# Kernel optimization log

Measured on AMD Instinct MI355X. Metric: run time of the kernel, lower is better.

Reference implementation:

```python
import jax, jax.numpy as jnp
import numpy as np

T_STEPS, B, DX, DH = 512, 64, 1024, 1024


def setup_inputs() -> dict:
    key = jax.random.key(0)
    ks = jax.random.split(key, 8)
    s_in = 1.0 / np.sqrt(DX)
    s_h = 1.0 / np.sqrt(DH)
    return {
        "xs": jax.random.normal(ks[0], (T_STEPS, B, DX), jnp.float32),
        "ms": jax.random.normal(ks[1], (T_STEPS, B, DH), jnp.float32),
        "h0": jnp.zeros((B, DH), jnp.float32),
        "W_ih": jax.random.normal(ks[2], (3 * DH, DX), jnp.float32) * s_in,
        "b_ih": jnp.zeros((3 * DH,), jnp.float32),
        "W_hh": jax.random.normal(ks[3], (3 * DH, DH), jnp.float32) * s_h,
        "b_hh": jnp.zeros((3 * DH,), jnp.float32),
        "W_xh": jax.random.normal(ks[4], (DH, DX), jnp.float32) * s_in,
        "b_xh": jnp.zeros((DH,), jnp.float32),
        "W_r": jax.random.normal(ks[5], (DH, DH), jnp.float32) * s_h,
        "b_r": jnpp if False else jnp.zeros((DH,), jnp.float32),
    }


def reference(xs, ms, h0, W_ih, b_ih, W_hh, b_hh, W_xh, b_xh, W_r, b_r):
    # Precompute all input-side projections in one big GEMM each (same math,
    # just hoisted out of the recurrent loop).
    xg = jnp.einsum('tbd,gd->tbg', xs, W_ih) + b_ih          # [T,B,3*Dh]
    xh = jnp.einsum('tbd,hd->tbh', xs, W_xh) + b_xh          # [T,B,Dh]
    tm = jnp.tanh(ms)                                        # [T,B,Dh]

    def step(h, inp):
        xg_t, xh_t, tm_t = inp
        hg = h @ W_hh.T + b_hh                               # [B,3*Dh]
        gates = jax.nn.sigmoid(xg_t + hg)
        rt, zt, et = jnp.split(gates, 3, axis=-1)
        ht_hat = jnp.tanh(xh_t + (rt * h) @ W_r.T + b_r)
        ht = zt * h + (1.0 - zt) * ht_hat + et * tm_t
        return ht, ht

    h_last, outs = jax.lax.scan(step, h0, (xg, xh, tm))
    return outs, h_last
```

## Files before the change

### kernel.cpp

```cpp
#include <hip/hip_runtime.h>
#include <stdint.h>

#define TSTEPS 512

typedef __attribute__((ext_vector_type(8))) _Float16 half8;
typedef __attribute__((ext_vector_type(4))) _Float16 half4;
typedef __attribute__((ext_vector_type(4))) float f32x4;
typedef __attribute__((ext_vector_type(4))) float float4v;
typedef __attribute__((ext_vector_type(4))) int i32x4;
typedef unsigned long long u64;

static __device__ __forceinline__ float sigm(float x) { return 1.f / (1.f + __expf(-x)); }
static __device__ __forceinline__ float tanh_(float x) {
  x = fminf(15.f, fmaxf(-15.f, x));
  float e = __expf(-2.f * x);
  return (1.f - e) / (1.f + e);
}
static __device__ __forceinline__ half8 ld8(const _Float16* p) { return *(const half8*)p; }
static __device__ __forceinline__ f32x4 MFMA(half8 a, half8 b, f32x4 c) {
  return __builtin_amdgcn_mfma_f32_16x16x32_f16(a, b, c, 0, 0, 0);
}
static __device__ __forceinline__ void pin8(half8& v) {
  i32x4 t = __builtin_bit_cast(i32x4, v);
  asm volatile("" : "+v"(t));
  v = __builtin_bit_cast(half8, t);
}

struct U64x2 { u64 x, y; };
static __device__ __forceinline__ half8 ld_msg16(const u64* p) {
  u64 a = __hip_atomic_load(p,     __ATOMIC_RELAXED, __HIP_MEMORY_SCOPE_AGENT);
  u64 b = __hip_atomic_load(p + 1, __ATOMIC_RELAXED, __HIP_MEMORY_SCOPE_AGENT);
  U64x2 u{a, b};
  return __builtin_bit_cast(half8, u);
}
static __device__ __forceinline__ void st_msg(u64* p, u64 v) {
  __hip_atomic_store(p, v, __ATOMIC_RELAXED, __HIP_MEMORY_SCOPE_AGENT);
}
static __device__ __forceinline__ void wait_flags(const unsigned* line, unsigned tag) {
  const unsigned* p = line + (threadIdx.x & 31);
  while (!__all(__hip_atomic_load(p, __ATOMIC_RELAXED, __HIP_MEMORY_SCOPE_AGENT) >= tag))
    __builtin_amdgcn_s_sleep(1);
  asm volatile("" ::: "memory");
}

__global__ __launch_bounds__(256) void kconv(
    const float* __restrict__ xs, const float* __restrict__ wih,
    const float* __restrict__ wxh, const float* __restrict__ whhf,
    const float* __restrict__ wrf, const float* __restrict__ h0,
    _Float16* __restrict__ xs_h, _Float16* __restrict__ wcat,
    _Float16* __restrict__ whh, _Float16* __restrict__ wr,
    _Float16* __restrict__ hx) {
  const long n1 = 8388608;
  const long n2 = 1048576;
  const long n3 = 786432;
  const long n4 = 262144;
  const long n5 = 16384;
  const long total = n1 + n2 + n3 + n4 + n5;
  for (long i = (long)blockIdx.x * 256 + threadIdx.x; i < total; i += (long)gridDim.x * 256) {
    const float* s; _Float16* d;
    if (i < n1) { s = xs + i * 4; d = xs_h + i * 4; }
    else if (i < n1 + n2) {
      long e = (i - n1) * 4;
      s = (e < 3145728) ? (wih + e) : (wxh + (e - 3145728));
      d = wcat + e;
    } else if (i < n1 + n2 + n3) { long e = (i - n1 - n2) * 4; s = whhf + e; d = whh + e; }
    else if (i < n1 + n2 + n3 + n4) { long e = (i - n1 - n2 - n3) * 4; s = wrf + e; d = wr + e; }
    else { long e = (i - n1 - n2 - n3 - n4) * 4; s = h0 + e; d = hx + e; }
    float4v v = *(const float4v*)s;
    half4 o = { (_Float16)v.x, (_Float16)v.y, (_Float16)v.z, (_Float16)v.w };
    *(half4*)d = o;
  }
}

__global__ __launch_bounds__(256) void kgemm(
    const _Float16* __restrict__ X, const _Float16* __restrict__ W,
    const float* __restrict__ b_ih, const float* __restrict__ b_xh,
    _Float16* __restrict__ C) {
  __shared__ _Float16 As[128 * 40], Bs[128 * 40];
  const int tid = threadIdx.x;
  const int lane = tid & 63;
  const int w = tid >> 6;
  const int wm = (w >> 1) * 64, wn = (w & 1) * 64;
  const int bn = blockIdx.x * 128;
  const int bm = blockIdx.y * 128;
  const int arow = tid >> 2;
  const int kk8 = (tid & 3) * 8;
  const int fr = lane & 15, fq = lane >> 4;
  const f32x4 zero = {0.f, 0.f, 0.f, 0.f};
  f32x4 acc[4][4];
  #pragma unroll
  for (int a = 0; a < 4; a++)
    #pragma unroll
    for (int b = 0; b < 4; b++) acc[a][b] = zero;
  for (int kt = 0; kt < 1024; kt += 32) {
    __syncthreads();
    #pragma unroll
    for (int j = 0; j < 2; j++) {
      int r = j * 64 + arow;
      *(half8*)(As + r * 40 + kk8) = ld8(X + (size_t)(bm + r) * 1024 + kt + kk8);
      *(half8*)(Bs + r * 40 + kk8) = ld8(W + (size_t)(bn + r) * 1024 + kt + kk8);
    }
    __syncthreads();
    half8 af[4], bfr[4];
    #pragma unroll
    for (int i = 0; i < 4; i++) {
      af[i]  = *(const half8*)(As + (wm + i * 16 + fr) * 40 + fq * 8);
      bfr[i] = *(const half8*)(Bs + (wn + i * 16 + fr) * 40 + fq * 8);
    }
    #pragma unroll
    for (int mi = 0; mi < 4; mi++)
      #pragma unroll
      for (int ni = 0; ni < 4; ni++)
        acc[mi][ni] = MFMA(af[mi], bfr[ni], acc[mi][ni]);
  }
  #pragma unroll
  for (int mi = 0; mi < 4; mi++)
    #pragma unroll
    for (int ni = 0; ni < 4; ni++) {
      int col = bn + wn + ni * 16 + fr;
      float bias = (col < 3072) ? b_ih[col] : b_xh[col - 3072];
      #pragma unroll
      for (int r = 0; r < 4; r++) {
        int row = bm + wm + mi * 16 + fq * 4 + r;
        C[(size_t)row * 4096 + col] = (_Float16)(acc[mi][ni][r] + bias);
      }
    }
}

#define RP 20
#define TP (16 * RP)

__global__ __launch_bounds__(512, 2) void krec(
    const _Float16* __restrict__ xgh, const float* __restrict__ ms,
    const _Float16* __restrict__ whh, const _Float16* __restrict__ wr,
    const float* __restrict__ b_hh, const float* __restrict__ b_r,
    const float* __restrict__ h0,
    u64* __restrict__ hmsg, u64* __restrict__ rhmsg,
    float* __restrict__ out, unsigned* __restrict__ ctr) {
  __shared__ float red[48 * TP];
  const int tid = threadIdx.x;
  const int lane = tid & 63, w = tid >> 6;
  const int fr = lane & 15, fq = lane >> 4;
  const int g = (int)blockIdx.x >> 5;
  const int slot = (int)blockIdx.x & 31;
  const int colbase = slot * 32;
  unsigned* flagA = ctr + (g * 2 + 0) * 32;
  unsigned* flagB = ctr + (g * 2 + 1) * 32;

  half8 wA[6][4], wB[2][4];
  #pragma unroll
  for (int nt = 0; nt < 6; nt++)
    #pragma unroll
    for (int ks = 0; ks < 4; ks++)
      wA[nt][ks] = ld8(whh + (size_t)((nt >> 1) * 1024 + colbase + (nt & 1) * 16 + fr) * 1024
                            + w * 128 + ks * 32 + fq * 8);
  #pragma unroll
  for (int nt = 0; nt < 2; nt++)
    #pragma unroll
    for (int ks = 0; ks < 4; ks++)
      wB[nt][ks] = ld8(wr + (size_t)(colbase + nt * 16 + fr) * 1024
                           + w * 128 + ks * 32 + fq * 8);
  #pragma unroll
  for (int nt = 0; nt < 6; nt++)
    #pragma unroll
    for (int ks = 0; ks < 4; ks++) pin8(wA[nt][ks]);
  #pragma unroll
  for (int nt = 0; nt < 2; nt++)
    #pragma unroll
    for (int ks = 0; ks < 4; ks++) pin8(wB[nt][ks]);

  const int b = tid >> 5, cc = tid & 31;
  const int gc = colbase + cc;
  const int gm = g * 16 + b;
  const float bhr = b_hh[gc], bhz = b_hh[1024 + gc], bhe = b_hh[2048 + gc];
  const float brr = b_r[gc];
  float hreg = h0[(size_t)gm * 1024 + gc];

  const u64* hcons = hmsg  + (g * 16 + fr) * 256 + w * 32 + fq * 2;
  const u64* rcons = rhmsg + (g * 16 + fr) * 256 + w * 32 + fq * 2;
  u64* hprod = hmsg  + gm * 256 + (gc >> 2);
  u64* rprod = rhmsg + gm * 256 + (gc >> 2);

  const f32x4 zero = {0.f, 0.f, 0.f, 0.f};

  float pxr, pxz, pxe, pxh, ptm;
  {
    const _Float16* xp = xgh + (size_t)gm * 4096;
    pxr = (float)xp[gc]; pxz = (float)xp[1024 + gc];
    pxe = (float)xp[2048 + gc]; pxh = (float)xp[3072 + gc];
    ptm = tanh_(ms[(size_t)gm * 1024 + gc]);
  }

  #pragma clang loop unroll(disable)
  for (int t = 0; t < TSTEPS; t++) {
    const int ph = t & 1;
    wait_flags(flagB, (unsigned)t);
    half8 av[4];
    #pragma unroll
    for (int ks = 0; ks < 4; ks++)
      av[ks] = ld_msg16(hcons + ph * 16384 + ks * 8);
    f32x4 accA[6];
    #pragma unroll
    for (int nt = 0; nt < 6; nt++) accA[nt] = zero;
    #pragma unroll
    for (int ks = 0; ks < 4; ks++)
      #pragma unroll
      for (int nt = 0; nt < 6; nt++)
        accA[nt] = MFMA(av[ks], wA[nt][ks], accA[nt]);
    #pragma unroll
    for (int nt = 0; nt < 6; nt++)
      #pragma unroll
      for (int r = 0; r < 4; r++)
        red[(w * 6 + nt) * TP + (fq * 4 + r) * RP + fr] = accA[nt][r];
    __syncthreads();
    float sr = pxr + bhr, sz = pxz + bhz, se = pxe + bhe;
    {
      const int boff = b * RP + (cc & 15) + (cc >> 4) * TP;
      #pragma unroll
      for (int w8 = 0; w8 < 8; w8++) {
        const float* rp = red + w8 * 6 * TP + boff;
        sr += rp[0]; sz += rp[2 * TP]; se += rp[4 * TP];
      }
    }
    float rg = sigm(sr);
    float zz = sigm(sz), ee = sigm(se);
    {
      float rv = rg * hreg;
      unsigned us = (unsigned)(unsigned short)__builtin_bit_cast(unsigned short, (_Float16)rv);
      unsigned v01 = us | (((unsigned)__shfl_down((int)us, 1) & 0xFFFFu) << 16);
      unsigned v23 = (unsigned)__shfl_down((int)v01, 2);
      if (!(cc & 3))
        st_msg(rprod + ph * 16384, ((u64)v23 << 32) | (u64)v01);
    }
    asm volatile("s_waitcnt vmcnt(0)" ::: "memory");
    __syncthreads();
    if (tid == 0)
      __hip_atomic_store(flagA + slot, (unsigned)(t + 1),
                         __ATOMIC_RELAXED, __HIP_MEMORY_SCOPE_AGENT);
    float nxr = 0.f, nxz = 0.f, nxe = 0.f, nxh = 0.f, ntm = 0.f;
    if (t + 1 < TSTEPS) {
      const _Float16* xp = xgh + (size_t)((t + 1) * 64 + gm) * 4096;
      nxr = (float)xp[gc]; nxz = (float)xp[1024 + gc];
      nxe = (float)xp[2048 + gc]; nxh = (float)xp[3072 + gc];
      ntm = tanh_(ms[(size_t)(t + 1) * 65536 + gm * 1024 + gc]);
    }

    wait_flags(flagA, (unsigned)(t + 1));
    half8 bv[4];
    #pragma unroll
    for (int ks = 0; ks < 4; ks++)
      bv[ks] = ld_msg16(rcons + ph * 16384 + ks * 8);
    f32x4 accB[2];
    #pragma unroll
    for (int nt = 0; nt < 2; nt++) accB[nt] = zero;
    #pragma unroll
    for (int ks = 0; ks < 4; ks++)
      #pragma unroll
      for (int nt = 0; nt < 2; nt++)
        accB[nt] = MFMA(bv[ks], wB[nt][ks], accB[nt]);
    #pragma unroll
    for (int nt = 0; nt < 2; nt++)
      #pragma unroll
      for (int r = 0; r < 4; r++)
        red[(w * 6 + nt) * TP + (fq * 4 + r) * RP + fr] = accB[nt][r];
    __syncthreads();
    float s = pxh + brr;
    {
      const int boff = b * RP + (cc & 15) + (cc >> 4) * TP;
      #pragma unroll
      for (int w8 = 0; w8 < 8; w8++) s += red[w8 * 6 * TP + boff];
    }
    float hh = tanh_(s);
    float hn = zz * hreg + (1.f - zz) * hh + ee * ptm;
    hreg = hn;
    {
      unsigned us = (unsigned)(unsigned short)__builtin_bit_cast(unsigned short, (_Float16)hn);
      unsigned v01 = us | (((unsigned)__shfl_down((int)us, 1) & 0xFFFFu) << 16);
      unsigned v23 = (unsigned)__shfl_down((int)v01, 2);
      if (!(cc & 3))
        st_msg(hprod + (ph ^ 1) * 16384, ((u64)v23 << 32) | (u64)v01);
    }
    asm volatile("s_waitcnt vmcnt(0)" ::: "memory");
    __syncthreads();
    if (tid == 0)
      __hip_atomic_store(flagB + slot, (unsigned)(t + 1),
                         __ATOMIC_RELAXED, __HIP_MEMORY_SCOPE_AGENT);
    __builtin_nontemporal_store(hn, out + (size_t)t * 65536 + gm * 1024 + gc);
    pxr = nxr; pxz = nxz; pxe = nxe; pxh = nxh; ptm = ntm;
  }
  out[(size_t)TSTEPS * 65536 + gm * 1024 + gc] = hreg;
}

extern "C" void kernel_launch(void* const* d_in, const int* in_sizes, int n_in,
                              void* d_out, int out_size, void* d_ws, size_t ws_size,
                              hipStream_t stream) {
  const float* xs   = (const float*)d_in[0];
  const float* ms   = (const float*)d_in[1];
  const float* h0   = (const float*)d_in[2];
  const float* W_ih = (const float*)d_in[3];
  const float* b_ih = (const float*)d_in[4];
  const float* W_hh = (const float*)d_in[5];
  const float* b_hh = (const float*)d_in[6];
  const float* W_xh = (const float*)d_in[7];
  const float* b_xh = (const float*)d_in[8];
  const float* W_r  = (const float*)d_in[9];
  const float* b_r  = (const float*)d_in[10];

  char* ws = (char*)d_ws;
  size_t off = 0;
  _Float16* xs_h = (_Float16*)(ws + off); off += 67108864;
  _Float16* wcat = (_Float16*)(ws + off); off += 8388608;
  _Float16* whh  = (_Float16*)(ws + off); off += 6291456;
  _Float16* wr   = (_Float16*)(ws + off); off += 2097152;
  _Float16* xgh  = (_Float16*)(ws + off); off += 268435456;
  _Float16* hx   = (_Float16*)(ws + off); off += 262144;
  _Float16* rhx  = (_Float16*)(ws + off); off += 262144;
  unsigned* ctr  = (unsigned*)(ws + off); off += 1024;

  hipMemsetAsync(ctr, 0, 1024, stream);
  kconv<<<2048, 256, 0, stream>>>(xs, W_ih, W_xh, W_hh, W_r, h0,
                                  xs_h, wcat, whh, wr, hx);
  kgemm<<<dim3(32, 256), 256, 0, stream>>>(xs_h, wcat, b_ih, b_xh, xgh);
  krec<<<128, 512, 0, stream>>>(xgh, ms, whh, wr, b_hh, b_r, h0,
                                (u64*)hx, (u64*)rhx, (float*)d_out, ctr);
}
```

Measured before the change: 4.455 ms.

## Place recurrent groups by XCC and exchange state through L2 atomics

The recurrent kernel now launches 256 blocks. Each block reads its XCC id and registers per XCC, so each 32-block group sits on one XCC and can exchange hidden-state messages and flags through that XCC's local L2 using atomic swap/add instructions instead of agent-scope loads. A global 'truth' flag acts as a fallback, and if placement fails the kernel falls back to the old global path. The first step also reads h0 directly instead of converting it in kconv, and the register pinning of weights is removed. This aims to cut cross-XCC coherence latency per timestep, at the cost of a startup rendezvous, spin-loop complexity and reliance on hardware-specific placement.

```diff
diff --git a/kernel.cpp b/kernel.cpp
--- a/kernel.cpp
+++ b/kernel.cpp
@@ -20,42 +20,62 @@
 static __device__ __forceinline__ f32x4 MFMA(half8 a, half8 b, f32x4 c) {
   return __builtin_amdgcn_mfma_f32_16x16x32_f16(a, b, c, 0, 0, 0);
 }
-static __device__ __forceinline__ void pin8(half8& v) {
-  i32x4 t = __builtin_bit_cast(i32x4, v);
-  asm volatile("" : "+v"(t));
-  v = __builtin_bit_cast(half8, t);
-}
-
-struct U64x2 { u64 x, y; };
-static __device__ __forceinline__ half8 ld_msg16(const u64* p) {
-  u64 a = __hip_atomic_load(p,     __ATOMIC_RELAXED, __HIP_MEMORY_SCOPE_AGENT);
-  u64 b = __hip_atomic_load(p + 1, __ATOMIC_RELAXED, __HIP_MEMORY_SCOPE_AGENT);
-  U64x2 u{a, b};
-  return __builtin_bit_cast(half8, u);
-}
-static __device__ __forceinline__ void st_msg(u64* p, u64 v) {
+
+static __device__ __forceinline__ unsigned aadd(unsigned* p) {
+  return __hip_atomic_fetch_add(p, 1u, __ATOMIC_RELAXED, __HIP_MEMORY_SCOPE_AGENT);
+}
+static __device__ __forceinline__ unsigned ald(const unsigned* p) {
+  return __hip_atomic_load(p, __ATOMIC_RELAXED, __HIP_MEMORY_SCOPE_AGENT);
+}
+static __device__ __forceinline__ void ast(unsigned* p, unsigned v) {
   __hip_atomic_store(p, v, __ATOMIC_RELAXED, __HIP_MEMORY_SCOPE_AGENT);
 }
-static __device__ __forceinline__ void wait_flags(const unsigned* line, unsigned tag) {
-  const unsigned* p = line + (threadIdx.x & 31);
-  while (!__all(__hip_atomic_load(p, __ATOMIC_RELAXED, __HIP_MEMORY_SCOPE_AGENT) >= tag))
-    __builtin_amdgcn_s_sleep(1);
-  asm volatile("" ::: "memory");
+static __device__ __forceinline__ u64 ald64(const u64* p) {
+  return __hip_atomic_load(p, __ATOMIC_RELAXED, __HIP_MEMORY_SCOPE_AGENT);
+}
+static __device__ __forceinline__ void ast64(u64* p, u64 v) {
+  __hip_atomic_store(p, v, __ATOMIC_RELAXED, __HIP_MEMORY_SCOPE_AGENT);
+}
+
+static __device__ __forceinline__ void l2_st64(u64* p, u64 v) {
+  asm volatile("global_atomic_swap_x2 %0, %1, off" :: "v"(p), "v"(v) : "memory");
+}
+static __device__ __forceinline__ void l2_st32(unsigned* p, unsigned v) {
+  asm volatile("global_atomic_swap %0, %1, off" :: "v"(p), "v"(v) : "memory");
+}
+static __device__ __forceinline__ unsigned l2_ld32(const unsigned* p) {
+  unsigned r, z = 0;
+  asm volatile("global_atomic_add %0, %1, %2, off sc0\n\ts_waitcnt vmcnt(0)"
+               : "=&v"(r) : "v"(p), "v"(z) : "memory");
+  return r;
+}
+static __device__ __forceinline__ void l2_ld_frag(
+    const u64* p0, const u64* p1, const u64* p2, const u64* p3, u64* m) {
+  u64 z = 0;
+  asm volatile(
+    "global_atomic_add_x2 %0, %8, %12, off sc0\n\t"
+    "global_atomic_add_x2 %1, %8, %12, off offset:8 sc0\n\t"
+    "global_atomic_add_x2 %2, %9, %12, off sc0\n\t"
+    "global_atomic_add_x2 %3, %9, %12, off offset:8 sc0\n\t"
+    "global_atomic_add_x2 %4, %10, %12, off sc0\n\t"
+    "global_atomic_add_x2 %5, %10, %12, off offset:8 sc0\n\t"
+    "global_atomic_add_x2 %6, %11, %12, off sc0\n\t"
+    "global_atomic_add_x2 %7, %11, %12, off offset:8 sc0\n\t"
+    "s_waitcnt vmcnt(0)"
+    : "=&v"(m[0]), "=&v"(m[1]), "=&v"(m[2]), "=&v"(m[3]),
+      "=&v"(m[4]), "=&v"(m[5]), "=&v"(m[6]), "=&v"(m[7])
+    : "v"(p0), "v"(p1), "v"(p2), "v"(p3), "v"(z)
+    : "memory");
 }
 
 __global__ __launch_bounds__(256) void kconv(
     const float* __restrict__ xs, const float* __restrict__ wih,
     const float* __restrict__ wxh, const float* __restrict__ whhf,
-    const float* __restrict__ wrf, const float* __restrict__ h0,
+    const float* __restrict__ wrf,
     _Float16* __restrict__ xs_h, _Float16* __restrict__ wcat,
-    _Float16* __restrict__ whh, _Float16* __restrict__ wr,
-    _Float16* __restrict__ hx) {
-  const long n1 = 8388608;
-  const long n2 = 1048576;
-  const long n3 = 786432;
-  const long n4 = 262144;
-  const long n5 = 16384;
-  const long total = n1 + n2 + n3 + n4 + n5;
+    _Float16* __restrict__ whh, _Float16* __restrict__ wr) {
+  const long n1 = 8388608, n2 = 1048576, n3 = 786432, n4 = 262144;
+  const long total = n1 + n2 + n3 + n4;
   for (long i = (long)blockIdx.x * 256 + threadIdx.x; i < total; i += (long)gridDim.x * 256) {
     const float* s; _Float16* d;
     if (i < n1) { s = xs + i * 4; d = xs_h + i * 4; }
@@ -64,8 +84,7 @@
       s = (e < 3145728) ? (wih + e) : (wxh + (e - 3145728));
       d = wcat + e;
     } else if (i < n1 + n2 + n3) { long e = (i - n1 - n2) * 4; s = whhf + e; d = whh + e; }
-    else if (i < n1 + n2 + n3 + n4) { long e = (i - n1 - n2 - n3) * 4; s = wrf + e; d = wr + e; }
-    else { long e = (i - n1 - n2 - n3 - n4) * 4; s = h0 + e; d = hx + e; }
+    else { long e = (i - n1 - n2 - n3) * 4; s = wrf + e; d = wr + e; }
     float4v v = *(const float4v*)s;
     half4 o = { (_Float16)v.x, (_Float16)v.y, (_Float16)v.z, (_Float16)v.w };
     *(half4*)d = o;
@@ -130,22 +149,50 @@
 #define RP 20
 #define TP (16 * RP)
 
-__global__ __launch_bounds__(512, 2) void krec(
+template<int LOCAL>
+static __device__ __forceinline__ void waitf(
+    const unsigned* fl, unsigned ftag, const unsigned* tr, unsigned ttag) {
+  if (LOCAL) {
+    if ((threadIdx.x >> 6) == 0) {
+      const unsigned* p = fl + (threadIdx.x & 31);
+      const unsigned* q = tr + (threadIdx.x & 31);
+      int it = 0;
+      for (;;) {
+        if (__all(l2_ld32(p) >= ftag)) break;
+        ++it;
+        if ((it & 63) == 0) {
+          if (__all(ald(q) >= ttag)) break;
+          if (it > 200000) break;
+        }
+        __builtin_amdgcn_s_sleep(1);
+      }
+    }
+    __syncthreads();
+  } else {
+    const unsigned* q = tr + (threadIdx.x & 31);
+    while (!__all(ald(q) >= ttag))
+      __builtin_amdgcn_s_sleep(1);
+  }
+  asm volatile("" ::: "memory");
+}
+
+template<int LOCAL>
+static __device__ void run_rec(
+    int tid, int grp, int slot, unsigned base,
     const _Float16* __restrict__ xgh, const float* __restrict__ ms,
     const _Float16* __restrict__ whh, const _Float16* __restrict__ wr,
     const float* __restrict__ b_hh, const float* __restrict__ b_r,
     const float* __restrict__ h0,
-    u64* __restrict__ hmsg, u64* __restrict__ rhmsg,
-    float* __restrict__ out, unsigned* __restrict__ ctr) {
-  __shared__ float red[48 * TP];
-  const int tid = threadIdx.x;
+    u64* __restrict__ hx, u64* __restrict__ rhx,
+    unsigned* __restrict__ truth, unsigned* __restrict__ flagsL,
+    float* __restrict__ out, float* red) {
   const int lane = tid & 63, w = tid >> 6;
   const int fr = lane & 15, fq = lane >> 4;
-  const int g = (int)blockIdx.x >> 5;
-  const int slot = (int)blockIdx.x & 31;
   const int colbase = slot * 32;
-  unsigned* flagA = ctr + (g * 2 + 0) * 32;
-  unsigned* flagB = ctr + (g * 2 + 1) * 32;
+  unsigned* flA = flagsL + grp * 64;
+  unsigned* flB = flagsL + grp * 64 + 32;
+  unsigned* trA = truth + grp * 64;
+  unsigned* trB = truth + grp * 64 + 32;
 
   half8 wA[6][4], wB[2][4];
   #pragma unroll
@@ -160,26 +207,18 @@
     for (int ks = 0; ks < 4; ks++)
       wB[nt][ks] = ld8(wr + (size_t)(colbase + nt * 16 + fr) * 1024
                            + w * 128 + ks * 32 + fq * 8);
-  #pragma unroll
-  for (int nt = 0; nt < 6; nt++)
-    #pragma unroll
-    for (int ks = 0; ks < 4; ks++) pin8(wA[nt][ks]);
-  #pragma unroll
-  for (int nt = 0; nt < 2; nt++)
-    #pragma unroll
-    for (int ks = 0; ks < 4; ks++) pin8(wB[nt][ks]);
 
   const int b = tid >> 5, cc = tid & 31;
   const int gc = colbase + cc;
-  const int gm = g * 16 + b;
+  const int gm = grp * 16 + b;
   const float bhr = b_hh[gc], bhz = b_hh[1024 + gc], bhe = b_hh[2048 + gc];
   const float brr = b_r[gc];
   float hreg = h0[(size_t)gm * 1024 + gc];
 
-  const u64* hcons = hmsg  + (g * 16 + fr) * 256 + w * 32 + fq * 2;
-  const u64* rcons = rhmsg + (g * 16 + fr) * 256 + w * 32 + fq * 2;
-  u64* hprod = hmsg  + gm * 256 + (gc >> 2);
-  u64* rprod = rhmsg + gm * 256 + (gc >> 2);
+  const u64* hcons = hx  + (size_t)(grp * 16 + fr) * 256 + w * 32 + fq * 2;
+  const u64* rcons = rhx + (size_t)(grp * 16 + fr) * 256 + w * 32 + fq * 2;
+  u64* hprod = hx  + (size_t)gm * 256 + (gc >> 2);
+  u64* rprod = rhx + (size_t)gm * 256 + (gc >> 2);
 
   const f32x4 zero = {0.f, 0.f, 0.f, 0.f};
 
@@ -194,11 +233,36 @@
   #pragma clang loop unroll(disable)
   for (int t = 0; t < TSTEPS; t++) {
     const int ph = t & 1;
-    wait_flags(flagB, (unsigned)t);
     half8 av[4];
-    #pragma unroll
-    for (int ks = 0; ks < 4; ks++)
-      av[ks] = ld_msg16(hcons + ph * 16384 + ks * 8);
+    if (t == 0) {
+      const float* hp = h0 + (size_t)(grp * 16 + fr) * 1024 + w * 128 + fq * 8;
+      #pragma unroll
+      for (int ks = 0; ks < 4; ks++) {
+        float4v a = *(const float4v*)(hp + ks * 32);
+        float4v c = *(const float4v*)(hp + ks * 32 + 4);
+        half8 h = { (_Float16)a.x, (_Float16)a.y, (_Float16)a.z, (_Float16)a.w,
+                    (_Float16)c.x, (_Float16)c.y, (_Float16)c.z, (_Float16)c.w };
+        av[ks] = h;
+      }
+    } else {
+      waitf<LOCAL>(flB, base + (unsigned)t, trB, (unsigned)t);
+      const u64* c0 = hcons + ph * 16384;
+      if (LOCAL) {
+        u64 m[8];
+        l2_ld_frag(c0, c0 + 8, c0 + 16, c0 + 24, m);
+        #pragma unroll
+        for (int ks = 0; ks < 4; ks++) {
+          struct { u64 a, b; } u{m[2 * ks], m[2 * ks + 1]};
+          av[ks] = __builtin_bit_cast(half8, u);
+        }
+      } else {
+        #pragma unroll
+        for (int ks = 0; ks < 4; ks++) {
+          struct { u64 a, b; } u{ald64(c0 + ks * 8), ald64(c0 + ks * 8 + 1)};
+          av[ks] = __builtin_bit_cast(half8, u);
+        }
+      }
+    }
     f32x4 accA[6];
     #pragma unroll
     for (int nt = 0; nt < 6; nt++) accA[nt] = zero;
@@ -229,15 +293,19 @@
       unsigned us = (unsigned)(unsigned short)__builtin_bit_cast(unsigned short, (_Float16)rv);
       unsigned v01 = us | (((unsigned)__shfl_down((int)us, 1) & 0xFFFFu) << 16);
       unsigned v23 = (unsigned)__shfl_down((int)v01, 2);
-      if (!(cc & 3))
-        st_msg(rprod + ph * 16384, ((u64)v23 << 32) | (u64)v01);
+      if (!(cc & 3)) {
+        u64 pv = ((u64)v23 << 32) | (u64)v01;
+        if (LOCAL) l2_st64(rprod + ph * 16384, pv);
+        else       ast64(rprod + ph * 16384, pv);
+      }
     }
     asm volatile("s_waitcnt vmcnt(0)" ::: "memory");
     __syncthreads();
-    if (tid == 0)
-      __hip_atomic_store(flagA + slot, (unsigned)(t + 1),
-                         __ATOMIC_RELAXED, __HIP_MEMORY_SCOPE_AGENT);
-    float nxr = 0.f, nxz = 0.f, nxe = 0.f, nxh = 0.f, ntm = 0.f;
+    if (tid == 0) {
+      if (LOCAL) l2_st32(flA + slot, base + (unsigned)(t + 1));
+      ast(trA + slot, (unsigned)(t + 1));
+    }
+    float nxr = 0, nxz = 0, nxe = 0, nxh = 0, ntm = 0;
     if (t + 1 < TSTEPS) {
       const _Float16* xp = xgh + (size_t)((t + 1) * 64 + gm) * 4096;
       nxr = (float)xp[gc]; nxz = (float)xp[1024 + gc];
@@ -245,11 +313,26 @@
       ntm = tanh_(ms[(size_t)(t + 1) * 65536 + gm * 1024 + gc]);
     }
 
-    wait_flags(flagA, (unsigned)(t + 1));
+    waitf<LOCAL>(flA, base + (unsigned)(t + 1), trA, (unsigned)(t + 1));
     half8 bv[4];
-    #pragma unroll
-    for (int ks = 0; ks < 4; ks++)
-      bv[ks] = ld_msg16(rcons + ph * 16384 + ks * 8);
+    {
+      const u64* c0 = rcons + ph * 16384;
+      if (LOCAL) {
+        u64 m[8];
+        l2_ld_frag(c0, c0 + 8, c0 + 16, c0 + 24, m);
+        #pragma unroll
+        for (int ks = 0; ks < 4; ks++) {
+          struct { u64 a, b; } u{m[2 * ks], m[2 * ks + 1]};
+          bv[ks] = __builtin_bit_cast(half8, u);
+        }
+      } else {
+        #pragma unroll
+        for (int ks = 0; ks < 4; ks++) {
+          struct { u64 a, b; } u{ald64(c0 + ks * 8), ald64(c0 + ks * 8 + 1)};
+          bv[ks] = __builtin_bit_cast(half8, u);
+        }
+      }
+    }
     f32x4 accB[2];
     #pragma unroll
     for (int nt = 0; nt < 2; nt++) accB[nt] = zero;
@@ -277,18 +360,86 @@
       unsigned us = (unsigned)(unsigned short)__builtin_bit_cast(unsigned short, (_Float16)hn);
       unsigned v01 = us | (((unsigned)__shfl_down((int)us, 1) & 0xFFFFu) << 16);
       unsigned v23 = (unsigned)__shfl_down((int)v01, 2);
-      if (!(cc & 3))
-        st_msg(hprod + (ph ^ 1) * 16384, ((u64)v23 << 32) | (u64)v01);
+      if (!(cc & 3)) {
+        u64 pv = ((u64)v23 << 32) | (u64)v01;
+        if (LOCAL) l2_st64(hprod + (ph ^ 1) * 16384, pv);
+        else       ast64(hprod + (ph ^ 1) * 16384, pv);
+      }
     }
     asm volatile("s_waitcnt vmcnt(0)" ::: "memory");
     __syncthreads();
-    if (tid == 0)
-      __hip_atomic_store(flagB + slot, (unsigned)(t + 1),
-                         __ATOMIC_RELAXED, __HIP_MEMORY_SCOPE_AGENT);
+    if (tid == 0) {
+      if (LOCAL) l2_st32(flB + slot, base + (unsigned)(t + 1));
+      ast(trB + slot, (unsigned)(t + 1));
+    }
     __builtin_nontemporal_store(hn, out + (size_t)t * 65536 + gm * 1024 + gc);
     pxr = nxr; pxz = nxz; pxe = nxe; pxh = nxh; ptm = ntm;
   }
   out[(size_t)TSTEPS * 65536 + gm * 1024 + gc] = hreg;
+}
+
+__global__ __launch_bounds__(512, 2) void krec(
+    const _Float16* __restrict__ xgh, const float* __restrict__ ms,
+    const _Float16* __restrict__ whh, const _Float16* __restrict__ wr,
+    const float* __restrict__ b_hh, const float* __restrict__ b_r,
+    const float* __restrict__ h0,
+    u64* __restrict__ hx, u64* __restrict__ rhx,
+    float* __restrict__ out, unsigned* __restrict__ ctr,
+    unsigned* __restrict__ flagsL) {
+  __shared__ float red[48 * TP];
+  __shared__ int sh[2];
+  __shared__ unsigned bsh;
+  const int tid = threadIdx.x;
+  unsigned* reg = ctr;
+  unsigned* truth = ctr + 64;
+
+  if (tid == 0) {
+    unsigned x;
+    asm volatile("s_getreg_b32 %0, hwreg(HW_REG_XCC_ID)" : "=s"(x));
+    x &= 7u;
+    unsigned slot = aadd(&reg[x]);
+    asm volatile("s_waitcnt vmcnt(0)" ::: "memory");
+    aadd(&reg[8]);
+    unsigned cnt = 0;
+    for (long it = 0; it < 4000000; ++it) {
+      cnt = ald(&reg[8]);
+      if (cnt >= 256u) break;
+      __builtin_amdgcn_s_sleep(8);
+    }
+    int ok = (cnt >= 256u);
+    if (ok)
+      #pragma unroll
+      for (int i = 0; i < 8; i++) ok &= (ald(&reg[i]) == 32u);
+    sh[0] = ok; sh[1] = (int)(x * 32u + (slot & 31u));
+  }
+  __syncthreads();
+
+  if (sh[0]) {
+    const int grp = sh[1] >> 5, slot = sh[1] & 31;
+    if (grp >= 4) return;
+    unsigned v = 0;
+    if (tid < 64) v = l2_ld32(flagsL + grp * 64 + tid);
+    if (tid == 0) bsh = 0;
+    __syncthreads();
+    if (tid < 64) atomicMax(&bsh, v);
+    __syncthreads();
+    const unsigned base = bsh;
+    if (tid == 0) {
+      aadd(&reg[9]);
+      for (long it = 0; it < 4000000; ++it) {
+        if (ald(&reg[9]) >= 128u) break;
+        __builtin_amdgcn_s_sleep(8);
+      }
+    }
+    __syncthreads();
+    run_rec<1>(tid, grp, slot, base, xgh, ms, whh, wr, b_hh, b_r, h0,
+               hx, rhx, truth, flagsL, out, red);
+  } else {
+    const int bid = (int)blockIdx.x;
+    if (bid >= 128) return;
+    run_rec<0>(tid, bid >> 5, bid & 31, 0u, xgh, ms, whh, wr, b_hh, b_r, h0,
+               hx, rhx, truth, flagsL, out, red);
+  }
 }
 
 extern "C" void kernel_launch(void* const* d_in, const int* in_sizes, int n_in,
@@ -313,14 +464,15 @@
   _Float16* whh  = (_Float16*)(ws + off); off += 6291456;
   _Float16* wr   = (_Float16*)(ws + off); off += 2097152;
   _Float16* xgh  = (_Float16*)(ws + off); off += 268435456;
-  _Float16* hx   = (_Float16*)(ws + off); off += 262144;
-  _Float16* rhx  = (_Float16*)(ws + off); off += 262144;
-  unsigned* ctr  = (unsigned*)(ws + off); off += 1024;
-
-  hipMemsetAsync(ctr, 0, 1024, stream);
-  kconv<<<2048, 256, 0, stream>>>(xs, W_ih, W_xh, W_hh, W_r, h0,
-                                  xs_h, wcat, whh, wr, hx);
+  u64* hx   = (u64*)(ws + off); off += 262144;
+  u64* rhx  = (u64*)(ws + off); off += 262144;
+  unsigned* ctr = (unsigned*)(ws + off); off += 4096;
+  unsigned* flagsL = (unsigned*)(ws + off); off += 4096;
+
+  hipMemsetAsync(ctr, 0, 4096, stream);
+  kconv<<<2048, 256, 0, stream>>>(xs, W_ih, W_xh, W_hh, W_r,
+                                  xs_h, wcat, whh, wr);
   kgemm<<<dim3(32, 256), 256, 0, stream>>>(xs_h, wcat, b_ih, b_xh, xgh);
-  krec<<<128, 512, 0, stream>>>(xgh, ms, whh, wr, b_hh, b_r, h0,
-                                (u64*)hx, (u64*)rhx, (float*)d_out, ctr);
-}
+  krec<<<256, 512, 0, stream>>>(xgh, ms, whh, wr, b_hh, b_r, h0,
+                                hx, rhx, (float*)d_out, ctr, flagsL);
+}
```

New measurement: 14.97 ms. 3.36x slower.

## Fuse input-projection GEMM into recurrent kernel with per-row-block readiness flags

Applied to the files above, without the earlier changes.

Merges the separate input GEMM launch into the persistent recurrent kernel: 128 blocks run the recurrence while another 128 blocks compute the xg/xh GEMM tiles in time order, bumping a per-row-block ready counter after write-through stores. Recurrent blocks spin on the counter before loading each step's projections, so the GEMM overlaps the serial recurrence instead of preceding it. It also drops the register-pinning asm on the weights. Risks include co-residency deadlock if the GEMM blocks cannot all be scheduled, extra LDS per block, and contention from the GEMM slowing the latency-bound recurrence.

```diff
diff --git a/kernel.cpp b/kernel.cpp
--- a/kernel.cpp
+++ b/kernel.cpp
@@ -7,7 +7,6 @@
 typedef __attribute__((ext_vector_type(4))) _Float16 half4;
 typedef __attribute__((ext_vector_type(4))) float f32x4;
 typedef __attribute__((ext_vector_type(4))) float float4v;
-typedef __attribute__((ext_vector_type(4))) int i32x4;
 typedef unsigned long long u64;
 
 static __device__ __forceinline__ float sigm(float x) { return 1.f / (1.f + __expf(-x)); }
@@ -20,12 +19,16 @@
 static __device__ __forceinline__ f32x4 MFMA(half8 a, half8 b, f32x4 c) {
   return __builtin_amdgcn_mfma_f32_16x16x32_f16(a, b, c, 0, 0, 0);
 }
-static __device__ __forceinline__ void pin8(half8& v) {
-  i32x4 t = __builtin_bit_cast(i32x4, v);
-  asm volatile("" : "+v"(t));
-  v = __builtin_bit_cast(half8, t);
-}
-
+
+static __device__ __forceinline__ unsigned aadd(unsigned* p) {
+  return __hip_atomic_fetch_add(p, 1u, __ATOMIC_RELAXED, __HIP_MEMORY_SCOPE_AGENT);
+}
+static __device__ __forceinline__ unsigned ald(const unsigned* p) {
+  return __hip_atomic_load(p, __ATOMIC_RELAXED, __HIP_MEMORY_SCOPE_AGENT);
+}
+static __device__ __forceinline__ void ast(unsigned* p, unsigned v) {
+  __hip_atomic_store(p, v, __ATOMIC_RELAXED, __HIP_MEMORY_SCOPE_AGENT);
+}
 struct U64x2 { u64 x, y; };
 static __device__ __forceinline__ half8 ld_msg16(const u64* p) {
   u64 a = __hip_atomic_load(p,     __ATOMIC_RELAXED, __HIP_MEMORY_SCOPE_AGENT);
@@ -38,9 +41,17 @@
 }
 static __device__ __forceinline__ void wait_flags(const unsigned* line, unsigned tag) {
   const unsigned* p = line + (threadIdx.x & 31);
-  while (!__all(__hip_atomic_load(p, __ATOMIC_RELAXED, __HIP_MEMORY_SCOPE_AGENT) >= tag))
+  while (!__all(ald(p) >= tag))
     __builtin_amdgcn_s_sleep(1);
   asm volatile("" ::: "memory");
+}
+static __device__ __forceinline__ void wait_blk(const unsigned* r) {
+  while (ald(r) < 32u) __builtin_amdgcn_s_sleep(4);
+  asm volatile("" ::: "memory");
+}
+static __device__ __forceinline__ void st_f16_wt(_Float16* p, float v) {
+  unsigned u = (unsigned)(unsigned short)__builtin_bit_cast(unsigned short, (_Float16)v);
+  asm volatile("global_store_short %0, %1, off sc0 sc1" :: "v"(p), "v"(u) : "memory");
 }
 
 __global__ __launch_bounds__(256) void kconv(
@@ -72,77 +83,88 @@
   }
 }
 
-__global__ __launch_bounds__(256) void kgemm(
+static __device__ void run_gemm(
+    int tid, int gw,
     const _Float16* __restrict__ X, const _Float16* __restrict__ W,
     const float* __restrict__ b_ih, const float* __restrict__ b_xh,
-    _Float16* __restrict__ C) {
-  __shared__ _Float16 As[128 * 40], Bs[128 * 40];
-  const int tid = threadIdx.x;
-  const int lane = tid & 63;
-  const int w = tid >> 6;
-  const int wm = (w >> 1) * 64, wn = (w & 1) * 64;
-  const int bn = blockIdx.x * 128;
-  const int bm = blockIdx.y * 128;
-  const int arow = tid >> 2;
-  const int kk8 = (tid & 3) * 8;
+    _Float16* __restrict__ C, unsigned* __restrict__ ready,
+    _Float16* As, _Float16* Bs) {
+  const int half = tid >> 8;
+  const int htid = tid & 255;
+  const int lane = htid & 63;
+  const int w4 = htid >> 6;
+  const int wm = (w4 >> 1) * 64, wn = (w4 & 1) * 64;
+  const int arow = htid >> 2;
+  const int kk8 = (htid & 3) * 8;
   const int fr = lane & 15, fq = lane >> 4;
+  _Float16* as = As + half * 5120;
+  _Float16* bs = Bs + half * 5120;
   const f32x4 zero = {0.f, 0.f, 0.f, 0.f};
-  f32x4 acc[4][4];
-  #pragma unroll
-  for (int a = 0; a < 4; a++)
-    #pragma unroll
-    for (int b = 0; b < 4; b++) acc[a][b] = zero;
-  for (int kt = 0; kt < 1024; kt += 32) {
-    __syncthreads();
-    #pragma unroll
-    for (int j = 0; j < 2; j++) {
-      int r = j * 64 + arow;
-      *(half8*)(As + r * 40 + kk8) = ld8(X + (size_t)(bm + r) * 1024 + kt + kk8);
-      *(half8*)(Bs + r * 40 + kk8) = ld8(W + (size_t)(bn + r) * 1024 + kt + kk8);
-    }
-    __syncthreads();
-    half8 af[4], bfr[4];
-    #pragma unroll
-    for (int i = 0; i < 4; i++) {
-      af[i]  = *(const half8*)(As + (wm + i * 16 + fr) * 40 + fq * 8);
-      bfr[i] = *(const half8*)(Bs + (wn + i * 16 + fr) * 40 + fq * 8);
+
+  for (int i = 0; i < 32; ++i) {
+    const int j = gw * 2 + half + 256 * i;
+    const int bm = j >> 5, bn = j & 31;
+    const int rb = bm * 128, cb = bn * 128;
+    f32x4 acc[4][4];
+    #pragma unroll
+    for (int a = 0; a < 4; a++)
+      #pragma unroll
+      for (int b = 0; b < 4; b++) acc[a][b] = zero;
+    for (int kt = 0; kt < 1024; kt += 32) {
+      __syncthreads();
+      #pragma unroll
+      for (int jj = 0; jj < 2; jj++) {
+        int r = jj * 64 + arow;
+        *(half8*)(as + r * 40 + kk8) = ld8(X + (size_t)(rb + r) * 1024 + kt + kk8);
+        *(half8*)(bs + r * 40 + kk8) = ld8(W + (size_t)(cb + r) * 1024 + kt + kk8);
+      }
+      __syncthreads();
+      half8 af[4], bfr[4];
+      #pragma unroll
+      for (int q = 0; q < 4; q++) {
+        af[q]  = *(const half8*)(as + (wm + q * 16 + fr) * 40 + fq * 8);
+        bfr[q] = *(const half8*)(bs + (wn + q * 16 + fr) * 40 + fq * 8);
+      }
+      #pragma unroll
+      for (int mi = 0; mi < 4; mi++)
+        #pragma unroll
+        for (int ni = 0; ni < 4; ni++)
+          acc[mi][ni] = MFMA(af[mi], bfr[ni], acc[mi][ni]);
     }
     #pragma unroll
     for (int mi = 0; mi < 4; mi++)
       #pragma unroll
-      for (int ni = 0; ni < 4; ni++)
-        acc[mi][ni] = MFMA(af[mi], bfr[ni], acc[mi][ni]);
-  }
-  #pragma unroll
-  for (int mi = 0; mi < 4; mi++)
-    #pragma unroll
-    for (int ni = 0; ni < 4; ni++) {
-      int col = bn + wn + ni * 16 + fr;
-      float bias = (col < 3072) ? b_ih[col] : b_xh[col - 3072];
-      #pragma unroll
-      for (int r = 0; r < 4; r++) {
-        int row = bm + wm + mi * 16 + fq * 4 + r;
-        C[(size_t)row * 4096 + col] = (_Float16)(acc[mi][ni][r] + bias);
+      for (int ni = 0; ni < 4; ni++) {
+        int col = cb + wn + ni * 16 + fr;
+        float bias = (col < 3072) ? b_ih[col] : b_xh[col - 3072];
+        #pragma unroll
+        for (int r = 0; r < 4; r++) {
+          int row = rb + wm + mi * 16 + fq * 4 + r;
+          st_f16_wt(C + (size_t)row * 4096 + col, acc[mi][ni][r] + bias);
+        }
       }
-    }
+    asm volatile("s_waitcnt vmcnt(0)" ::: "memory");
+    __syncthreads();
+    if (htid == 0) (void)aadd(&ready[bm]);
+  }
 }
 
 #define RP 20
 #define TP (16 * RP)
 
-__global__ __launch_bounds__(512, 2) void krec(
+static __device__ void run_rec(
+    int tid, int bid,
     const _Float16* __restrict__ xgh, const float* __restrict__ ms,
     const _Float16* __restrict__ whh, const _Float16* __restrict__ wr,
     const float* __restrict__ b_hh, const float* __restrict__ b_r,
     const float* __restrict__ h0,
     u64* __restrict__ hmsg, u64* __restrict__ rhmsg,
-    float* __restrict__ out, unsigned* __restrict__ ctr) {
-  __shared__ float red[48 * TP];
-  const int tid = threadIdx.x;
+    float* __restrict__ out, unsigned* __restrict__ ctr,
+    unsigned* __restrict__ ready, float* red) {
   const int lane = tid & 63, w = tid >> 6;
   const int fr = lane & 15, fq = lane >> 4;
-  const int g = (int)blockIdx.x >> 5;
-  const int slot = (int)blockIdx.x & 31;
+  const int g = bid >> 5;
+  const int slot = bid & 31;
   const int colbase = slot * 32;
   unsigned* flagA = ctr + (g * 2 + 0) * 32;
   unsigned* flagB = ctr + (g * 2 + 1) * 32;
@@ -160,14 +182,6 @@
     for (int ks = 0; ks < 4; ks++)
       wB[nt][ks] = ld8(wr + (size_t)(colbase + nt * 16 + fr) * 1024
                            + w * 128 + ks * 32 + fq * 8);
-  #pragma unroll
-  for (int nt = 0; nt < 6; nt++)
-    #pragma unroll
-    for (int ks = 0; ks < 4; ks++) pin8(wA[nt][ks]);
-  #pragma unroll
-  for (int nt = 0; nt < 2; nt++)
-    #pragma unroll
-    for (int ks = 0; ks < 4; ks++) pin8(wB[nt][ks]);
 
   const int b = tid >> 5, cc = tid & 31;
   const int gc = colbase + cc;
@@ -184,6 +198,7 @@
   const f32x4 zero = {0.f, 0.f, 0.f, 0.f};
 
   float pxr, pxz, pxe, pxh, ptm;
+  wait_blk(&ready[0]);
   {
     const _Float16* xp = xgh + (size_t)gm * 4096;
     pxr = (float)xp[gc]; pxz = (float)xp[1024 + gc];
@@ -235,17 +250,17 @@
     asm volatile("s_waitcnt vmcnt(0)" ::: "memory");
     __syncthreads();
     if (tid == 0)
-      __hip_atomic_store(flagA + slot, (unsigned)(t + 1),
-                         __ATOMIC_RELAXED, __HIP_MEMORY_SCOPE_AGENT);
+      ast(flagA + slot, (unsigned)(t + 1));
     float nxr = 0.f, nxz = 0.f, nxe = 0.f, nxh = 0.f, ntm = 0.f;
     if (t + 1 < TSTEPS) {
+      wait_blk(&ready[(t + 1) >> 1]);
       const _Float16* xp = xgh + (size_t)((t + 1) * 64 + gm) * 4096;
       nxr = (float)xp[gc]; nxz = (float)xp[1024 + gc];
       nxe = (float)xp[2048 + gc]; nxh = (float)xp[3072 + gc];
       ntm = tanh_(ms[(size_t)(t + 1) * 65536 + gm * 1024 + gc]);
     }
-
     wait_flags(flagA, (unsigned)(t + 1));
+
     half8 bv[4];
     #pragma unroll
     for (int ks = 0; ks < 4; ks++)
@@ -283,12 +298,35 @@
     asm volatile("s_waitcnt vmcnt(0)" ::: "memory");
     __syncthreads();
     if (tid == 0)
-      __hip_atomic_store(flagB + slot, (unsigned)(t + 1),
-                         __ATOMIC_RELAXED, __HIP_MEMORY_SCOPE_AGENT);
+      ast(flagB + slot, (unsigned)(t + 1));
     __builtin_nontemporal_store(hn, out + (size_t)t * 65536 + gm * 1024 + gc);
     pxr = nxr; pxz = nxz; pxe = nxe; pxh = nxh; ptm = ntm;
   }
   out[(size_t)TSTEPS * 65536 + gm * 1024 + gc] = hreg;
+}
+
+__global__ __launch_bounds__(512, 2) void krec(
+    const _Float16* __restrict__ xgh_c, const float* __restrict__ ms,
+    const _Float16* __restrict__ whh, const _Float16* __restrict__ wr,
+    const float* __restrict__ b_hh, const float* __restrict__ b_r,
+    const float* __restrict__ h0,
+    u64* __restrict__ hmsg, u64* __restrict__ rhmsg,
+    float* __restrict__ out, unsigned* __restrict__ ctr,
+    const _Float16* __restrict__ X, const _Float16* __restrict__ W,
+    const float* __restrict__ b_ih, const float* __restrict__ b_xh,
+    _Float16* __restrict__ xgh_w) {
+  __shared__ float red[48 * TP];
+  __shared__ _Float16 As[2 * 5120], Bs[2 * 5120];
+  const int tid = threadIdx.x;
+  const int bid = (int)blockIdx.x;
+  unsigned* ready = ctr + 256;
+
+  if (bid < 128) {
+    run_rec(tid, bid, xgh_c, ms, whh, wr, b_hh, b_r, h0,
+            hmsg, rhmsg, out, ctr, ready, red);
+  } else {
+    run_gemm(tid, bid - 128, X, W, b_ih, b_xh, xgh_w, ready, As, Bs);
+  }
 }
 
 extern "C" void kernel_launch(void* const* d_in, const int* in_sizes, int n_in,
@@ -315,12 +353,12 @@
   _Float16* xgh  = (_Float16*)(ws + off); off += 268435456;
   _Float16* hx   = (_Float16*)(ws + off); off += 262144;
   _Float16* rhx  = (_Float16*)(ws + off); off += 262144;
-  unsigned* ctr  = (unsigned*)(ws + off); off += 1024;
-
-  hipMemsetAsync(ctr, 0, 1024, stream);
+  unsigned* ctr  = (unsigned*)(ws + off); off += 2048;
+
+  hipMemsetAsync(ctr, 0, 2048, stream);
   kconv<<<2048, 256, 0, stream>>>(xs, W_ih, W_xh, W_hh, W_r, h0,
                                   xs_h, wcat, whh, wr, hx);
-  kgemm<<<dim3(32, 256), 256, 0, stream>>>(xs_h, wcat, b_ih, b_xh, xgh);
-  krec<<<128, 512, 0, stream>>>(xgh, ms, whh, wr, b_hh, b_r, h0,
-                                (u64*)hx, (u64*)rhx, (float*)d_out, ctr);
-}
+  krec<<<256, 512, 0, stream>>>(xgh, ms, whh, wr, b_hh, b_r, h0,
+                                (u64*)hx, (u64*)rhx, (float*)d_out, ctr,
+                                xs_h, wcat, b_ih, b_xh, xgh);
+}
```

Measured after the change: 4.317 ms. 3.1% less time.
